# Kernel optimization log

Measured on AMD Instinct MI355X. Metric: run time of the kernel, lower is better.

## Reference

```python
import jax, jax.numpy as jnp
import numpy as np

THRESH = 0.5
SCALE_POS = 2.0
SCALE_NEG = 40.0


def setup_inputs() -> dict:
    key = jax.random.key(0)
    k1, k2, k3, k4 = jax.random.split(key, 4)
    N, M, D, C = 8192, 8192, 256, 100
    emb_img = jax.random.normal(k1, (N, D), dtype=jnp.float32)
    emb_text = jax.random.normal(k2, (M, D), dtype=jnp.float32)
    # L2-normalize: cosine similarities in [-1,1], as the thresh/scale values assume
    emb_img = emb_img / jnp.linalg.norm(emb_img, axis=-1, keepdims=True)
    emb_text = emb_text / jnp.linalg.norm(emb_text, axis=-1, keepdims=True)
    gt_pre = jax.random.randint(k3, (N,), 0, C, dtype=jnp.int64 if jax.config.jax_enable_x64 else jnp.int32).astype(jnp.int32)
    gt_pres_map = jax.random.randint(k4, (M,), 0, C, dtype=jnp.int32)
    return {"emb_img": emb_img, "emb_text": emb_text, "gt_pre": gt_pre, "gt_pres_map": gt_pres_map}


def reference(emb_img, emb_text, gt_pre, gt_pres_map):
    # [N, M] pairwise similarity
    matrix = jnp.matmul(emb_img, emb_text.T)
    # vectorized equivalent of the nested python loop: z[i,j] = (gt_pre[i] == gt_pres_map[j])
    z = gt_pre[:, None] == gt_pres_map[None, :]
    # matrix_p = z*matrix; kept entries are where z==1 AND matrix>0 (same for negatives with 1-z)
    pos_mask = z & (matrix > 0)
    neg_mask = (~z) & (matrix > 0)
    pos_cnt = jnp.sum(pos_mask)
    neg_cnt = jnp.sum(neg_mask)
    pos_sum = jnp.sum(jnp.where(pos_mask, jnp.exp(-SCALE_POS * (matrix - THRESH)), 0.0))
    neg_sum = jnp.sum(jnp.where(neg_mask, jnp.exp(SCALE_NEG * (matrix - THRESH)), 0.0))
    pos_loss = jnp.where(
        pos_cnt > 0,
        jnp.log1p(pos_sum) / (SCALE_POS * jnp.maximum(pos_cnt, 1).astype(matrix.dtype)),
        jnp.zeros((), matrix.dtype),
    )
    neg_loss = jnp.where(
        neg_cnt > 0,
        jnp.log1p(neg_sum) / (SCALE_NEG * jnp.maximum(neg_cnt, 1).astype(matrix.dtype)),
        jnp.zeros((), matrix.dtype),
    )
    return pos_loss + neg_loss
```

## Files before the change

### kernel.cpp

```cpp
#include <hip/hip_runtime.h>
#include <hip/hip_bf16.h>
#include <math.h>

#define N_IMG 8192
#define M_TXT 8192
#define DIMK  256
#define BT    128
#define BK    32

typedef short bf16x8 __attribute__((ext_vector_type(8)));
typedef float f32x4  __attribute__((ext_vector_type(4)));

__device__ inline void gload_lds16(const void* g, void* l) {
    __builtin_amdgcn_global_load_lds(
        (const __attribute__((address_space(1))) unsigned int*)g,
        (__attribute__((address_space(3))) unsigned int*)l,
        16, 0, 0);
}

__device__ inline unsigned short f2bf(float x) {
    unsigned u = __float_as_uint(x);
    u += 0x7FFFu + ((u >> 16) & 1u);
    return (unsigned short)(u >> 16);
}

__global__ void convert_swz(const float* __restrict__ srcA,
                            const float* __restrict__ srcB,
                            unsigned short* __restrict__ dstA,
                            unsigned short* __restrict__ dstB,
                            double* __restrict__ accums) {
    if (blockIdx.x == 0) {
#pragma unroll
        for (int s = 0; s < 8; ++s) accums[threadIdx.x * 8 + s] = 0.0;
    }
    int q = blockIdx.x * blockDim.x + threadIdx.x;
    const int per = N_IMG * (DIMK / 8);
    const float* src; unsigned short* dst; int qq = q;
    if (q < per) { src = srcA; dst = dstA; }
    else         { src = srcB; dst = dstB; qq = q - per; }
    int r  = qq >> 5, jj = qq & 31;
    int kb = jj >> 2, j = jj & 3;
    int c  = (j - (r >> 1)) & 3;
    const float4* s = (const float4*)(src + (size_t)r * DIMK + kb * 32 + c * 8);
    float4 a = s[0], b = s[1];
    uint4 w;
    w.x = (unsigned)f2bf(a.x) | ((unsigned)f2bf(a.y) << 16);
    w.y = (unsigned)f2bf(a.z) | ((unsigned)f2bf(a.w) << 16);
    w.z = (unsigned)f2bf(b.x) | ((unsigned)f2bf(b.y) << 16);
    w.w = (unsigned)f2bf(b.z) | ((unsigned)f2bf(b.w) << 16);
    ((uint4*)dst)[qq] = w;
}

__launch_bounds__(256, 3)
__global__ void msloss_gemm(const unsigned short* __restrict__ Abf,
                            const unsigned short* __restrict__ Bbf,
                            const int* __restrict__ rowLab,
                            const int* __restrict__ colLab,
                            double* __restrict__ accums) {
    __shared__ __align__(16) unsigned short As[2][BT * BK];
    __shared__ __align__(16) unsigned short Bs[2][BT * BK];

    int tid  = threadIdx.x;
    int wave = tid >> 6, lane = tid & 63;
    int r16  = lane & 15, kg = lane >> 4;
    int wrow = (wave >> 1) * 64, wcol = (wave & 1) * 64;

    int swz = (blockIdx.x & 7) * 512 + (blockIdx.x >> 3);
    int tileRow = (swz >> 6) * BT;
    int tileCol = (swz & 63) * BT;

    auto STAGE = [&](int sel, int k0) {
#pragma unroll
        for (int i = 0; i < 2; ++i) {
            int p = wave * 128 + i * 64 + lane;
            int r = p >> 2, j = p & 3;
            gload_lds16(Abf + (size_t)(tileRow + r) * DIMK + k0 + j * 8,
                        &As[sel][(wave * 128 + i * 64) * 8]);
        }
#pragma unroll
        for (int i = 0; i < 2; ++i) {
            int p = wave * 128 + i * 64 + lane;
            int r = p >> 2, j = p & 3;
            gload_lds16(Bbf + (size_t)(tileCol + r) * DIMK + k0 + j * 8,
                        &Bs[sel][(wave * 128 + i * 64) * 8]);
        }
    };

    f32x4 acc[4][4] = {};

    STAGE(0, 0);
    asm volatile("s_waitcnt vmcnt(0)" ::: "memory");
    __builtin_amdgcn_s_barrier();
    __builtin_amdgcn_sched_barrier(0);

#pragma unroll 1
    for (int t = 0; t < DIMK / BK; ++t) {
        if (t < DIMK / BK - 1) {
            STAGE((t + 1) & 1, (t + 1) * BK);
            asm volatile("s_waitcnt vmcnt(4)" ::: "memory");
        } else {
            asm volatile("s_waitcnt vmcnt(0)" ::: "memory");
        }
        __builtin_amdgcn_s_barrier();
        __builtin_amdgcn_sched_barrier(0);

        const unsigned short* as = As[t & 1];
        const unsigned short* bs = Bs[t & 1];
        int slot = ((r16 >> 1) + kg) & 3;
        bf16x8 a[4], b[4];
#pragma unroll
        for (int m = 0; m < 4; ++m)
            a[m] = *(const bf16x8*)(as + (wrow + m * 16 + r16) * BK + slot * 8);
#pragma unroll
        for (int n = 0; n < 4; ++n)
            b[n] = *(const bf16x8*)(bs + (wcol + n * 16 + r16) * BK + slot * 8);
#pragma unroll
        for (int m = 0; m < 4; ++m)
#pragma unroll
            for (int n = 0; n < 4; ++n)
                acc[m][n] = __builtin_amdgcn_mfma_f32_16x16x32_bf16(
                    a[m], b[n], acc[m][n], 0, 0, 0);

        asm volatile("s_waitcnt lgkmcnt(0)" ::: "memory");
        __builtin_amdgcn_sched_barrier(0);
        __builtin_amdgcn_s_barrier();
    }

    int4 rl4[4]; int mycl[4];
#pragma unroll
    for (int m = 0; m < 4; ++m)
        rl4[m] = *(const int4*)(rowLab + tileRow + wrow + m * 16 + kg * 4);
#pragma unroll
    for (int n = 0; n < 4; ++n)
        mycl[n] = colLab[tileCol + wcol + n * 16 + r16];

    const float CPOS = -2.885390081777927f;
    const float CNEG = 57.707801635558536f;
    float ps = 0.f, ns = 0.f;
    int   pc = 0,   nc = 0;
#pragma unroll
    for (int m = 0; m < 4; ++m) {
        int lab[4] = {rl4[m].x, rl4[m].y, rl4[m].z, rl4[m].w};
#pragma unroll
        for (int j = 0; j < 4; ++j) {
            int myrl = lab[j];
#pragma unroll
            for (int n = 0; n < 4; ++n) {
                float v  = acc[m][n][j];
                bool eq  = (myrl == mycl[n]);
                bool pos = v > 0.f;
                float e  = exp2f((v - 0.5f) * (eq ? CPOS : CNEG));
                ps += (pos && eq)  ? e : 0.f;
                ns += (pos && !eq) ? e : 0.f;
                pc += (pos && eq)  ? 1 : 0;
                nc += (pos && !eq) ? 1 : 0;
            }
        }
    }
#pragma unroll
    for (int off = 32; off > 0; off >>= 1) {
        ps += __shfl_down(ps, off, 64);
        ns += __shfl_down(ns, off, 64);
        pc += __shfl_down(pc, off, 64);
        nc += __shfl_down(nc, off, 64);
    }
    if (lane == 0) {
        double* s = accums + ((((unsigned)blockIdx.x << 2) | (unsigned)wave) & 255u) * 8;
        atomicAdd(s + 0, (double)ps);
        atomicAdd(s + 1, (double)ns);
        atomicAdd((unsigned long long*)(s + 2), (unsigned long long)pc);
        atomicAdd((unsigned long long*)(s + 3), (unsigned long long)nc);
    }
}

__global__ void finalize_loss(const double* __restrict__ accums,
                              float* __restrict__ out) {
    int lane = threadIdx.x;
    double ps = 0, ns = 0, pc = 0, nc = 0;
#pragma unroll
    for (int s = lane; s < 256; s += 64) {
        ps += accums[s * 8 + 0];
        ns += accums[s * 8 + 1];
        pc += (double)((const unsigned long long*)accums)[s * 8 + 2];
        nc += (double)((const unsigned long long*)accums)[s * 8 + 3];
    }
#pragma unroll
    for (int off = 32; off > 0; off >>= 1) {
        ps += __shfl_down(ps, off, 64);
        ns += __shfl_down(ns, off, 64);
        pc += __shfl_down(pc, off, 64);
        nc += __shfl_down(nc, off, 64);
    }
    if (lane == 0) {
        double pl = (pc > 0.0) ? log1p(ps) / (2.0 * pc)  : 0.0;
        double nl = (nc > 0.0) ? log1p(ns) / (40.0 * nc) : 0.0;
        out[0] = (float)(pl + nl);
    }
}

extern "C" void kernel_launch(void* const* d_in, const int* in_sizes, int n_in,
                              void* d_out, int out_size, void* d_ws, size_t ws_size,
                              hipStream_t stream) {
    (void)in_sizes; (void)n_in; (void)out_size;
    const float* img    = (const float*)d_in[0];
    const float* txt    = (const float*)d_in[1];
    const int*   gt_pre = (const int*)d_in[2];
    const int*   gt_map = (const int*)d_in[3];
    float* out = (float*)d_out;

    const size_t ACC_BYTES = 256 * 8 * sizeof(double);
    const size_t MAT_BYTES = (size_t)N_IMG * DIMK * 2;
    if (ws_size < ACC_BYTES + 2 * MAT_BYTES) return;

    double*         accums = (double*)d_ws;
    unsigned short* Abf = (unsigned short*)((char*)d_ws + ACC_BYTES);
    unsigned short* Bbf = (unsigned short*)((char*)d_ws + ACC_BYTES + MAT_BYTES);

    int nchunks = 2 * N_IMG * (DIMK / 8);
    convert_swz<<<nchunks / 256, 256, 0, stream>>>(img, txt, Abf, Bbf, accums);
    msloss_gemm<<<(N_IMG / BT) * (M_TXT / BT), 256, 0, stream>>>(Abf, Bbf, gt_pre, gt_map, accums);
    finalize_loss<<<1, 64, 0, stream>>>(accums, out);
}
```

Before: 76.09 us.

## Switch to 32x32x16 MFMA tiles and restructure epilogue with ballot-based counting

Replaces the 16x16x32 bf16 MFMA with 32x32x16 instructions on 2x2 accumulator tiles, which changes the LDS fragment loads and the swizzled slot indexing to match. The epilogue computes the negative exponential for every positive entry and subtracts it back for positive pairs. It counts entries with wave ballots and popcounts, and evaluates the positive exp only when some lane in the wave has a label match. Occupancy is raised through launch bounds and MFMA priority is set around the inner product. Subtracting the exp sums may lose some precision. Setting launch bounds to 4 may force register spilling with the 16-wide accumulators.

Result: slower. 83.26 us (+9.4%).

```diff
diff --git a/kernel.cpp b/kernel.cpp
--- a/kernel.cpp
+++ b/kernel.cpp
@@ -9,7 +9,7 @@
 #define BK    32
 
 typedef short bf16x8 __attribute__((ext_vector_type(8)));
-typedef float f32x4  __attribute__((ext_vector_type(4)));
+typedef float f32x16 __attribute__((ext_vector_type(16)));
 
 __device__ inline void gload_lds16(const void* g, void* l) {
     __builtin_amdgcn_global_load_lds(
@@ -51,7 +51,7 @@
     ((uint4*)dst)[qq] = w;
 }
 
-__launch_bounds__(256, 3)
+__launch_bounds__(256, 4)
 __global__ void msloss_gemm(const unsigned short* __restrict__ Abf,
                             const unsigned short* __restrict__ Bbf,
                             const int* __restrict__ rowLab,
@@ -62,7 +62,7 @@
 
     int tid  = threadIdx.x;
     int wave = tid >> 6, lane = tid & 63;
-    int r16  = lane & 15, kg = lane >> 4;
+    int l31  = lane & 31, hi = lane >> 5;
     int wrow = (wave >> 1) * 64, wcol = (wave & 1) * 64;
 
     int swz = (blockIdx.x & 7) * 512 + (blockIdx.x >> 3);
@@ -86,12 +86,14 @@
         }
     };
 
-    f32x4 acc[4][4] = {};
+    f32x16 acc[2][2] = {};
 
     STAGE(0, 0);
     asm volatile("s_waitcnt vmcnt(0)" ::: "memory");
     __builtin_amdgcn_s_barrier();
     __builtin_amdgcn_sched_barrier(0);
+
+    int rot = (l31 >> 1) & 3;
 
 #pragma unroll 1
     for (int t = 0; t < DIMK / BK; ++t) {
@@ -106,70 +108,94 @@
 
         const unsigned short* as = As[t & 1];
         const unsigned short* bs = Bs[t & 1];
-        int slot = ((r16 >> 1) + kg) & 3;
-        bf16x8 a[4], b[4];
-#pragma unroll
-        for (int m = 0; m < 4; ++m)
-            a[m] = *(const bf16x8*)(as + (wrow + m * 16 + r16) * BK + slot * 8);
-#pragma unroll
-        for (int n = 0; n < 4; ++n)
-            b[n] = *(const bf16x8*)(bs + (wcol + n * 16 + r16) * BK + slot * 8);
-#pragma unroll
-        for (int m = 0; m < 4; ++m)
-#pragma unroll
-            for (int n = 0; n < 4; ++n)
-                acc[m][n] = __builtin_amdgcn_mfma_f32_16x16x32_bf16(
-                    a[m], b[n], acc[m][n], 0, 0, 0);
+        bf16x8 a[2][2], b[2][2];
+#pragma unroll
+        for (int mi = 0; mi < 2; ++mi)
+#pragma unroll
+            for (int ks = 0; ks < 2; ++ks) {
+                int slot = (ks * 2 + hi + rot) & 3;
+                a[mi][ks] = *(const bf16x8*)(as + (wrow + mi * 32 + l31) * BK + slot * 8);
+            }
+#pragma unroll
+        for (int ni = 0; ni < 2; ++ni)
+#pragma unroll
+            for (int ks = 0; ks < 2; ++ks) {
+                int slot = (ks * 2 + hi + rot) & 3;
+                b[ni][ks] = *(const bf16x8*)(bs + (wcol + ni * 32 + l31) * BK + slot * 8);
+            }
+
+        __builtin_amdgcn_s_setprio(1);
+#pragma unroll
+        for (int ks = 0; ks < 2; ++ks)
+#pragma unroll
+            for (int mi = 0; mi < 2; ++mi)
+#pragma unroll
+                for (int ni = 0; ni < 2; ++ni)
+                    acc[mi][ni] = __builtin_amdgcn_mfma_f32_32x32x16_bf16(
+                        a[mi][ks], b[ni][ks], acc[mi][ni], 0, 0, 0);
+        __builtin_amdgcn_s_setprio(0);
 
         asm volatile("s_waitcnt lgkmcnt(0)" ::: "memory");
         __builtin_amdgcn_sched_barrier(0);
         __builtin_amdgcn_s_barrier();
     }
 
-    int4 rl4[4]; int mycl[4];
-#pragma unroll
-    for (int m = 0; m < 4; ++m)
-        rl4[m] = *(const int4*)(rowLab + tileRow + wrow + m * 16 + kg * 4);
-#pragma unroll
-    for (int n = 0; n < 4; ++n)
-        mycl[n] = colLab[tileCol + wcol + n * 16 + r16];
-
-    const float CPOS = -2.885390081777927f;
+    int tr = tileRow + wrow, tc = tileCol + wcol;
+    int cl0 = colLab[tc + l31];
+    int cl1 = colLab[tc + 32 + l31];
+
     const float CNEG = 57.707801635558536f;
-    float ps = 0.f, ns = 0.f;
-    int   pc = 0,   nc = 0;
-#pragma unroll
-    for (int m = 0; m < 4; ++m) {
-        int lab[4] = {rl4[m].x, rl4[m].y, rl4[m].z, rl4[m].w};
-#pragma unroll
-        for (int j = 0; j < 4; ++j) {
-            int myrl = lab[j];
-#pragma unroll
-            for (int n = 0; n < 4; ++n) {
-                float v  = acc[m][n][j];
-                bool eq  = (myrl == mycl[n]);
-                bool pos = v > 0.f;
-                float e  = exp2f((v - 0.5f) * (eq ? CPOS : CNEG));
-                ps += (pos && eq)  ? e : 0.f;
-                ns += (pos && !eq) ? e : 0.f;
-                pc += (pos && eq)  ? 1 : 0;
-                nc += (pos && !eq) ? 1 : 0;
+    const float DNEG = -28.853900817779268f;
+    const float CPOS = -2.8853900817779268f;
+    const float DPOS = 1.4426950408889634f;
+
+    float ps = 0.f, nsa = 0.f, nsc = 0.f;
+    int posc = 0, pec = 0;
+
+#pragma unroll
+    for (int mi = 0; mi < 2; ++mi) {
+        int4 rl4[4];
+#pragma unroll
+        for (int g = 0; g < 4; ++g)
+            rl4[g] = *(const int4*)(rowLab + tr + mi * 32 + g * 8 + 4 * hi);
+#pragma unroll
+        for (int g = 0; g < 4; ++g) {
+            int lab[4] = {rl4[g].x, rl4[g].y, rl4[g].z, rl4[g].w};
+#pragma unroll
+            for (int j = 0; j < 4; ++j) {
+                int myrl = lab[j];
+#pragma unroll
+                for (int ni = 0; ni < 2; ++ni) {
+                    float v  = acc[mi][ni][g * 4 + j];
+                    bool pos = v > 0.f;
+                    bool eq  = myrl == (ni ? cl1 : cl0);
+                    float en = exp2f(fmaf(v, CNEG, DNEG));
+                    nsa += pos ? en : 0.f;
+                    posc += (int)__popcll(__ballot(pos));
+                    unsigned long long mpe = __ballot(pos && eq);
+                    if (mpe) {
+                        bool pe  = pos && eq;
+                        float ep = exp2f(fmaf(v, CPOS, DPOS));
+                        ps  += pe ? ep : 0.f;
+                        nsc += pe ? en : 0.f;
+                        pec += (int)__popcll(mpe);
+                    }
+                }
             }
         }
     }
+    float ns = nsa - nsc;
 #pragma unroll
     for (int off = 32; off > 0; off >>= 1) {
         ps += __shfl_down(ps, off, 64);
         ns += __shfl_down(ns, off, 64);
-        pc += __shfl_down(pc, off, 64);
-        nc += __shfl_down(nc, off, 64);
     }
     if (lane == 0) {
         double* s = accums + ((((unsigned)blockIdx.x << 2) | (unsigned)wave) & 255u) * 8;
         atomicAdd(s + 0, (double)ps);
         atomicAdd(s + 1, (double)ns);
-        atomicAdd((unsigned long long*)(s + 2), (unsigned long long)pc);
-        atomicAdd((unsigned long long*)(s + 3), (unsigned long long)nc);
+        atomicAdd((unsigned long long*)(s + 2), (unsigned long long)pec);
+        atomicAdd((unsigned long long*)(s + 3), (unsigned long long)(posc - pec));
     }
 }
 
```

## Triple-buffer LDS tiles, drop trailing barrier, hoist label loads, ballot-based counts

Applied to the files above, without the earlier changes.

Moves from two to three LDS stages so each iteration needs only one barrier. With three buffers the next prefetch never overwrites the tile being read, so the trailing lgkmcnt wait and second barrier are removed and the k-loop is fully unrolled. Label loads move before the GEMM so their latency overlaps with it. The epilogue folds the subtract into an fma and replaces the per-lane counters and their shuffle reductions with wave ballots and popcounts. The cost is more LDS per block, which could reduce occupancy at 3 blocks per CU.

New measurement: 78.90 us. 3.7% more time.

```diff
diff --git a/kernel.cpp b/kernel.cpp
--- a/kernel.cpp
+++ b/kernel.cpp
@@ -57,8 +57,8 @@
                             const int* __restrict__ rowLab,
                             const int* __restrict__ colLab,
                             double* __restrict__ accums) {
-    __shared__ __align__(16) unsigned short As[2][BT * BK];
-    __shared__ __align__(16) unsigned short Bs[2][BT * BK];
+    __shared__ __align__(16) unsigned short As[3][BT * BK];
+    __shared__ __align__(16) unsigned short Bs[3][BT * BK];
 
     int tid  = threadIdx.x;
     int wave = tid >> 6, lane = tid & 63;
@@ -68,6 +68,15 @@
     int swz = (blockIdx.x & 7) * 512 + (blockIdx.x >> 3);
     int tileRow = (swz >> 6) * BT;
     int tileCol = (swz & 63) * BT;
+
+    int tr = tileRow + wrow, tc = tileCol + wcol;
+    int4 rl4[4]; int mycl[4];
+#pragma unroll
+    for (int m = 0; m < 4; ++m)
+        rl4[m] = *(const int4*)(rowLab + tr + m * 16 + kg * 4);
+#pragma unroll
+    for (int n = 0; n < 4; ++n)
+        mycl[n] = colLab[tc + n * 16 + r16];
 
     auto STAGE = [&](int sel, int k0) {
 #pragma unroll
@@ -87,16 +96,14 @@
     };
 
     f32x4 acc[4][4] = {};
+    int slot = ((r16 >> 1) + kg) & 3;
 
     STAGE(0, 0);
-    asm volatile("s_waitcnt vmcnt(0)" ::: "memory");
-    __builtin_amdgcn_s_barrier();
-    __builtin_amdgcn_sched_barrier(0);
-
-#pragma unroll 1
+
+#pragma unroll 8
     for (int t = 0; t < DIMK / BK; ++t) {
         if (t < DIMK / BK - 1) {
-            STAGE((t + 1) & 1, (t + 1) * BK);
+            STAGE((t + 1) % 3, (t + 1) * BK);
             asm volatile("s_waitcnt vmcnt(4)" ::: "memory");
         } else {
             asm volatile("s_waitcnt vmcnt(0)" ::: "memory");
@@ -104,9 +111,8 @@
         __builtin_amdgcn_s_barrier();
         __builtin_amdgcn_sched_barrier(0);
 
-        const unsigned short* as = As[t & 1];
-        const unsigned short* bs = Bs[t & 1];
-        int slot = ((r16 >> 1) + kg) & 3;
+        const unsigned short* as = As[t % 3];
+        const unsigned short* bs = Bs[t % 3];
         bf16x8 a[4], b[4];
 #pragma unroll
         for (int m = 0; m < 4; ++m)
@@ -120,24 +126,15 @@
             for (int n = 0; n < 4; ++n)
                 acc[m][n] = __builtin_amdgcn_mfma_f32_16x16x32_bf16(
                     a[m], b[n], acc[m][n], 0, 0, 0);
-
-        asm volatile("s_waitcnt lgkmcnt(0)" ::: "memory");
-        __builtin_amdgcn_sched_barrier(0);
-        __builtin_amdgcn_s_barrier();
-    }
-
-    int4 rl4[4]; int mycl[4];
-#pragma unroll
-    for (int m = 0; m < 4; ++m)
-        rl4[m] = *(const int4*)(rowLab + tileRow + wrow + m * 16 + kg * 4);
-#pragma unroll
-    for (int n = 0; n < 4; ++n)
-        mycl[n] = colLab[tileCol + wcol + n * 16 + r16];
-
-    const float CPOS = -2.885390081777927f;
+    }
+
+    const float CPOS = -2.8853900817779268f;
     const float CNEG = 57.707801635558536f;
+    const float DPOS = 1.4426950408889634f;
+    const float DNEG = -28.853900817779268f;
+
     float ps = 0.f, ns = 0.f;
-    int   pc = 0,   nc = 0;
+    unsigned posc = 0, pec = 0;
 #pragma unroll
     for (int m = 0; m < 4; ++m) {
         int lab[4] = {rl4[m].x, rl4[m].y, rl4[m].z, rl4[m].w};
@@ -149,11 +146,11 @@
                 float v  = acc[m][n][j];
                 bool eq  = (myrl == mycl[n]);
                 bool pos = v > 0.f;
-                float e  = exp2f((v - 0.5f) * (eq ? CPOS : CNEG));
+                float e  = exp2f(fmaf(v, eq ? CPOS : CNEG, eq ? DPOS : DNEG));
                 ps += (pos && eq)  ? e : 0.f;
                 ns += (pos && !eq) ? e : 0.f;
-                pc += (pos && eq)  ? 1 : 0;
-                nc += (pos && !eq) ? 1 : 0;
+                posc += (unsigned)__popcll(__ballot(pos));
+                pec  += (unsigned)__popcll(__ballot(pos && eq));
             }
         }
     }
@@ -161,15 +158,13 @@
     for (int off = 32; off > 0; off >>= 1) {
         ps += __shfl_down(ps, off, 64);
         ns += __shfl_down(ns, off, 64);
-        pc += __shfl_down(pc, off, 64);
-        nc += __shfl_down(nc, off, 64);
     }
     if (lane == 0) {
         double* s = accums + ((((unsigned)blockIdx.x << 2) | (unsigned)wave) & 255u) * 8;
         atomicAdd(s + 0, (double)ps);
         atomicAdd(s + 1, (double)ns);
-        atomicAdd((unsigned long long*)(s + 2), (unsigned long long)pc);
-        atomicAdd((unsigned long long*)(s + 3), (unsigned long long)nc);
+        atomicAdd((unsigned long long*)(s + 2), (unsigned long long)pec);
+        atomicAdd((unsigned long long*)(s + 3), (unsigned long long)(posc - pec));
     }
 }
 
```
